# Performance work log

Measured on AMD Instinct MI355X. Metric: run time of the kernel, lower is better.

The kernel has to match this reference:

```python
import jax, jax.numpy as jnp
import numpy as np

N = 50          # n_nodes
TAU = 1.0       # sinkhorn_tau
ITERS = 5       # sinkhorn_iters
ALPHA = 1.0


def _psi_fn(x, W1, b1, W2, b2):
    # x: [B, N, F]
    h = jax.nn.leaky_relu(x @ W1 + b1)          # [B, N, H], slope 0.01 matches torch default
    M = jax.nn.leaky_relu(h @ W2 + b2)          # [B, N, N]
    P = jnp.exp(M / TAU)
    for _ in range(ITERS):                      # alternating row/col normalization
        P = P / jnp.sum(P, axis=2, keepdims=True)
        P = P / jnp.sum(P, axis=1, keepdims=True)
    return P


def _hungarian(cost):
    """O(n^3) Hungarian (shortest augmenting path, like scipy.linear_sum_assignment).
    cost: [n, n] numpy. Returns col index assigned to each row (minimizes cost)."""
    n = cost.shape[0]
    INF = 1e18
    u = np.zeros(n + 1)
    v = np.zeros(n + 1)
    p = np.zeros(n + 1, dtype=np.int64)   # p[j] = row matched to column j (1-based)
    for i in range(1, n + 1):
        p[0] = i
        j0 = 0
        minv = np.full(n + 1, INF)
        way = np.zeros(n + 1, dtype=np.int64)
        used = np.zeros(n + 1, dtype=bool)
        while True:
            used[j0] = True
            i0 = p[j0]
            cur = cost[i0 - 1, :] - u[i0] - v[1:]
            free = ~used[1:]
            better = free & (cur < minv[1:])
            mv = minv[1:]
            mv[better] = cur[better]
            way[1:][better] = j0
            cand = np.where(free, mv, INF)
            j1 = int(np.argmin(cand)) + 1
            delta = cand[j1 - 1]
            u[p[used]] += delta
            v[used] -= delta
            mv[free] -= delta
            j0 = j1
            if p[j0] == 0:
                break
        while j0 != 0:
            j1 = way[j0]
            p[j0] = p[j1]
            j0 = j1
    row_to_col = np.zeros(n, dtype=np.int64)
    for j in range(1, n + 1):
        if p[j] > 0:
            row_to_col[p[j] - 1] = j - 1
    return row_to_col


def setup_inputs() -> dict:
    key = jax.random.key(0)
    k1, k2, k3, k4, k5 = jax.random.split(key, 5)
    B, F, H = 128, 1024, 4096
    s1 = 1.0 / np.sqrt(F)
    s2 = 1.0 / np.sqrt(H)
    x = jax.random.normal(k1, (B, N, F), dtype=jnp.float32)
    W1 = jax.random.uniform(k2, (F, H), minval=-s1, maxval=s1, dtype=jnp.float32)
    b1 = jax.random.uniform(k3, (H,), minval=-s1, maxval=s1, dtype=jnp.float32)
    W2 = jax.random.uniform(k4, (H, N), minval=-s2, maxval=s2, dtype=jnp.float32)
    b2 = jax.random.uniform(k5, (N,), minval=-s2, maxval=s2, dtype=jnp.float32)
    return {"x": x, "W1": W1, "b1": b1, "W2": W2, "b2": b2, "do_round": 1}


def reference(x, W1, b1, W2, b2, do_round):
    psi = _psi_fn(x, W1, b1, W2, b2)            # [B, N, N] doubly-stochastic (approx)
    if do_round:
        batch = np.asarray(psi)
        B = batch.shape[0]
        perms_np = np.zeros((B, N, N), dtype=np.float32)
        rows = np.arange(N)
        for i in range(B):
            cols = _hungarian(-batch[i])        # maximize psi == minimize -psi
            perms_np[i, rows, cols] = 1.0
        perms = jnp.asarray(perms_np)
        dist = jnp.sum(psi * perms, axis=(1, 2)) / N   # [B]
        X = (1.0 - ALPHA) * perms + ALPHA * psi
        return (psi, perms, X, dist)
    return (psi, None, None, None)
```

## Files before the change

### kernel.cpp

```cpp
#include <hip/hip_runtime.h>

#define NMAT 50
#define BATCH 128
#define FDIM 1024
#define HDIM 4096
#define ROWS 6400
#define PSIZE 320000
#define NPART 8
#define HINF 1e18

#define WS_M_OFF   0
#define WS_XH_OFF  10240000LL
#define WS_XL_OFF  23347200LL
#define WS_W1H_OFF 36454400LL
#define WS_W1L_OFF 44843008LL
#define WS_W2H_OFF 53231616LL
#define WS_W2L_OFF 53755904LL
#define WS_H_OFF   54280192LL
#define WS_MIN     (WS_H_OFF + 128LL * HDIM * 4)

typedef __bf16 bf16x8 __attribute__((ext_vector_type(8)));
typedef short short8 __attribute__((ext_vector_type(8)));
typedef float f32x4 __attribute__((ext_vector_type(4)));
typedef unsigned short u16;
typedef unsigned int u32;

__device__ __forceinline__ float bf16_to_f32(unsigned short h) {
  return __uint_as_float(((unsigned int)h) << 16);
}
__device__ __forceinline__ unsigned short f32_to_bf16(float f) {
  unsigned int u = __float_as_uint(f);
  u += 0x7FFFu + ((u >> 16) & 1u);
  return (unsigned short)(u >> 16);
}

__device__ __forceinline__ void gload16(const u16* g, u16* l) {
  __builtin_amdgcn_global_load_lds(
      (const __attribute__((address_space(1))) unsigned int*)g,
      (__attribute__((address_space(3))) unsigned int*)l, 16, 0, 0);
}

__device__ __forceinline__ double wave_min_f64(double x) {
  union { double d; int i[2]; } u, t;
  u.d = x;
#define DPP_MIN_STEP(ctrl)                                                   \
  t.i[0] = __builtin_amdgcn_update_dpp(u.i[0], u.i[0], ctrl, 0xf, 0xf, false);\
  t.i[1] = __builtin_amdgcn_update_dpp(u.i[1], u.i[1], ctrl, 0xf, 0xf, false);\
  u.d = fmin(u.d, t.d);
  DPP_MIN_STEP(0x111)
  DPP_MIN_STEP(0x112)
  DPP_MIN_STEP(0x114)
  DPP_MIN_STEP(0x118)
  DPP_MIN_STEP(0x142)
  DPP_MIN_STEP(0x143)
#undef DPP_MIN_STEP
  union { double d; int i[2]; } r;
  r.i[0] = __builtin_amdgcn_readlane(u.i[0], 63);
  r.i[1] = __builtin_amdgcn_readlane(u.i[1], 63);
  return r.d;
}

__global__ __launch_bounds__(256) void convert_x(
    const float* __restrict__ X, u16* __restrict__ Xh, u16* __restrict__ Xl) {
  int t = threadIdx.x;
  int mt = blockIdx.x >> 5, k0b = blockIdx.x & 31;
  size_t outbase = (size_t)blockIdx.x * 4096;
#pragma unroll
  for (int it = 0; it < 2; ++it) {
    int idx = t + it * 256;
    int m = idx & 127, kg = idx >> 7;
    const float* src = X + (size_t)(mt * 128 + m) * FDIM + k0b * 32 + kg * 8;
    float4 v0 = *(const float4*)src;
    float4 v1 = *(const float4*)(src + 4);
    float f[8] = {v0.x, v0.y, v0.z, v0.w, v1.x, v1.y, v1.z, v1.w};
    unsigned short h[8], l[8];
#pragma unroll
    for (int j = 0; j < 8; ++j) {
      h[j] = f32_to_bf16(f[j]);
      l[j] = f32_to_bf16(f[j] - bf16_to_f32(h[j]));
    }
    uint4 hv, lv;
    hv.x = h[0] | ((unsigned)h[1] << 16); hv.y = h[2] | ((unsigned)h[3] << 16);
    hv.z = h[4] | ((unsigned)h[5] << 16); hv.w = h[6] | ((unsigned)h[7] << 16);
    lv.x = l[0] | ((unsigned)l[1] << 16); lv.y = l[2] | ((unsigned)l[3] << 16);
    lv.z = l[4] | ((unsigned)l[5] << 16); lv.w = l[6] | ((unsigned)l[7] << 16);
    size_t off = outbase + (size_t)(kg * 128 + m) * 8;
    *(uint4*)&Xh[off] = hv;
    *(uint4*)&Xl[off] = lv;
  }
}

__global__ __launch_bounds__(256) void convert_w1(
    const float* __restrict__ W1, u16* __restrict__ Wh, u16* __restrict__ Wl) {
  int t = threadIdx.x;
  int nt = blockIdx.x >> 5, k0b = blockIdx.x & 31;
  size_t outbase = (size_t)blockIdx.x * 4096;
#pragma unroll
  for (int it = 0; it < 2; ++it) {
    int idx = t + it * 256;
    int n = idx & 127, kg = idx >> 7;
    float f[8];
#pragma unroll
    for (int j = 0; j < 8; ++j)
      f[j] = W1[(size_t)(k0b * 32 + kg * 8 + j) * HDIM + nt * 128 + n];
    unsigned short h[8], l[8];
#pragma unroll
    for (int j = 0; j < 8; ++j) {
      h[j] = f32_to_bf16(f[j]);
      l[j] = f32_to_bf16(f[j] - bf16_to_f32(h[j]));
    }
    uint4 hv, lv;
    hv.x = h[0] | ((unsigned)h[1] << 16); hv.y = h[2] | ((unsigned)h[3] << 16);
    hv.z = h[4] | ((unsigned)h[5] << 16); hv.w = h[6] | ((unsigned)h[7] << 16);
    lv.x = l[0] | ((unsigned)l[1] << 16); lv.y = l[2] | ((unsigned)l[3] << 16);
    lv.z = l[4] | ((unsigned)l[5] << 16); lv.w = l[6] | ((unsigned)l[7] << 16);
    size_t off = outbase + (size_t)(kg * 128 + n) * 8;
    *(uint4*)&Wh[off] = hv;
    *(uint4*)&Wl[off] = lv;
  }
}

__global__ __launch_bounds__(256) void convert_w2(
    const float* __restrict__ W2, u16* __restrict__ W2h, u16* __restrict__ W2l) {
  int idx = blockIdx.x * 256 + threadIdx.x;
  int n = idx >> 12, k = idx & 4095;
  float f = (n < NMAT) ? W2[(size_t)k * NMAT + n] : 0.0f;
  unsigned short hi = f32_to_bf16(f);
  unsigned short lo = f32_to_bf16(f - bf16_to_f32(hi));
  W2h[idx] = hi;
  W2l[idx] = lo;
}

__global__ __launch_bounds__(256) void gemm1_mfma(
    const u16* __restrict__ Ah_, const u16* __restrict__ Al_,
    const u16* __restrict__ Bh_, const u16* __restrict__ Bl_,
    const float* __restrict__ b1,
    u32* __restrict__ HTout,
    int mt0, int stride) {
  __shared__ __align__(16) u16 Ah[4096];
  __shared__ __align__(16) u16 Al[4096];
  __shared__ __align__(16) u16 Bh[4096];
  __shared__ __align__(16) u16 Bl[4096];
  int t = threadIdx.x;
  int wave = t >> 6, lane = t & 63;
  int nt = blockIdx.x & 31;
  int mtl = blockIdx.x >> 5;
  int wm = wave >> 1, wn = wave & 1;
  int fr = lane & 15, fg = lane >> 4;

  f32x4 acc[4][4];
#pragma unroll
  for (int i = 0; i < 4; ++i)
#pragma unroll
    for (int j = 0; j < 4; ++j) acc[i][j] = (f32x4){0.f, 0.f, 0.f, 0.f};

  const u16* pAh = Ah_ + (size_t)(mt0 + mtl) * 32 * 4096;
  const u16* pAl = Al_ + (size_t)(mt0 + mtl) * 32 * 4096;
  const u16* pBh = Bh_ + (size_t)nt * 32 * 4096;
  const u16* pBl = Bl_ + (size_t)nt * 32 * 4096;
  int so = wave * 1024 + lane * 8;
  int ld = wave * 1024;

  for (int k0b = 0; k0b < 32; ++k0b) {
    __syncthreads();
    size_t sb = (size_t)k0b * 4096;
    gload16(pAh + sb + so,       &Ah[ld]);
    gload16(pAh + sb + so + 512, &Ah[ld + 512]);
    gload16(pAl + sb + so,       &Al[ld]);
    gload16(pAl + sb + so + 512, &Al[ld + 512]);
    gload16(pBh + sb + so,       &Bh[ld]);
    gload16(pBh + sb + so + 512, &Bh[ld + 512]);
    gload16(pBl + sb + so,       &Bl[ld]);
    gload16(pBl + sb + so + 512, &Bl[ld + 512]);
    __syncthreads();
    bf16x8 ah[4], al[4], bh[4], bl[4];
#pragma unroll
    for (int i = 0; i < 4; ++i) {
      int arow = (fg * 128 + wm * 64 + i * 16 + fr) * 8;
      ah[i] = *(const bf16x8*)&Ah[arow];
      al[i] = *(const bf16x8*)&Al[arow];
      int brow = (fg * 128 + wn * 64 + i * 16 + fr) * 8;
      bh[i] = *(const bf16x8*)&Bh[brow];
      bl[i] = *(const bf16x8*)&Bl[brow];
    }
#pragma unroll
    for (int i = 0; i < 4; ++i)
#pragma unroll
      for (int j = 0; j < 4; ++j)
        acc[i][j] = __builtin_amdgcn_mfma_f32_16x16x32_bf16(ah[i], bh[j], acc[i][j], 0, 0, 0);
#pragma unroll
    for (int i = 0; i < 4; ++i)
#pragma unroll
      for (int j = 0; j < 4; ++j)
        acc[i][j] = __builtin_amdgcn_mfma_f32_16x16x32_bf16(ah[i], bl[j], acc[i][j], 0, 0, 0);
#pragma unroll
    for (int i = 0; i < 4; ++i)
#pragma unroll
      for (int j = 0; j < 4; ++j)
        acc[i][j] = __builtin_amdgcn_mfma_f32_16x16x32_bf16(al[i], bh[j], acc[i][j], 0, 0, 0);
  }

  int colb = nt * 128 + wn * 64 + fr;
  int rowb = mtl * 128 + wm * 64 + fg * 4;
#pragma unroll
  for (int j = 0; j < 4; ++j) {
    float bias = b1[colb + j * 16];
#pragma unroll
    for (int i = 0; i < 4; ++i) {
      uint4 pk;
      u32* pp = &pk.x;
#pragma unroll
      for (int r = 0; r < 4; ++r) {
        float v = acc[i][j][r] + bias;
        v = v >= 0.0f ? v : 0.01f * v;
        unsigned short hi = f32_to_bf16(v);
        unsigned short lo = f32_to_bf16(v - bf16_to_f32(hi));
        pp[r] = ((u32)hi << 16) | lo;
      }
      *(uint4*)&HTout[(size_t)(colb + j * 16) * stride + rowb + i * 16] = pk;
    }
  }
}

__global__ __launch_bounds__(64) void gemm2_bf16(
    const u32* __restrict__ hT,
    const u16* __restrict__ W2h,
    const u16* __restrict__ W2l,
    float* __restrict__ Mpart,
    int row0, int stride) {
  int lane = threadIdx.x;
  int kz = blockIdx.y;
  int fr = lane & 15, fg = lane >> 4;

  f32x4 acc[4];
#pragma unroll
  for (int nt = 0; nt < 4; ++nt) acc[nt] = (f32x4){0.f, 0.f, 0.f, 0.f};

  const u32* hA = hT + blockIdx.x * 16 + fr;
  const int kbase = kz * 512;
  u32 hp[8];
#pragma unroll
  for (int kk = 0; kk < 8; ++kk)
    hp[kk] = hA[(size_t)(kbase + fg * 8 + kk) * stride];

  for (int ks = 0; ks < 16; ++ks) {
    int k0 = kbase + ks * 32;
    u32 hn[8];
    if (ks < 15) {
#pragma unroll
      for (int kk = 0; kk < 8; ++kk)
        hn[kk] = hA[(size_t)(k0 + 32 + fg * 8 + kk) * stride];
    }
    short8 hs, ls;
#pragma unroll
    for (int kk = 0; kk < 8; ++kk) {
      hs[kk] = (short)(hp[kk] >> 16);
      ls[kk] = (short)(hp[kk] & 0xffffu);
    }
    bf16x8 ah = *(bf16x8*)&hs;
    bf16x8 al = *(bf16x8*)&ls;
#pragma unroll
    for (int nt = 0; nt < 4; ++nt) {
      const size_t boff = (size_t)(nt * 16 + fr) * 4096 + k0 + fg * 8;
      bf16x8 bh = *(const bf16x8*)&W2h[boff];
      bf16x8 bl = *(const bf16x8*)&W2l[boff];
      acc[nt] = __builtin_amdgcn_mfma_f32_16x16x32_bf16(ah, bh, acc[nt], 0, 0, 0);
      acc[nt] = __builtin_amdgcn_mfma_f32_16x16x32_bf16(ah, bl, acc[nt], 0, 0, 0);
      acc[nt] = __builtin_amdgcn_mfma_f32_16x16x32_bf16(al, bh, acc[nt], 0, 0, 0);
    }
    if (ks < 15) {
#pragma unroll
      for (int kk = 0; kk < 8; ++kk) hp[kk] = hn[kk];
    }
  }

  float* Mout = Mpart + (size_t)kz * PSIZE;
  int rowbase = row0 + blockIdx.x * 16 + fg * 4;
#pragma unroll
  for (int nt = 0; nt < 4; ++nt) {
    int col = nt * 16 + fr;
    if (col < NMAT) {
#pragma unroll
      for (int r = 0; r < 4; ++r)
        Mout[(size_t)(rowbase + r) * NMAT + col] = acc[nt][r];
    }
  }
}

__global__ __launch_bounds__(64) void sinkhorn_hungarian(
    const float* __restrict__ Mpart, const float* __restrict__ b2,
    float* __restrict__ out_psi, float* __restrict__ out_X,
    float* __restrict__ out_perms, float* __restrict__ out_dist) {
  int b = blockIdx.x, lane = threadIdx.x;
  __shared__ double P[2500];
  __shared__ double cost[2500];
  __shared__ double rs[50];
  __shared__ double u[51];
  __shared__ int p[51];
  __shared__ int wayl[51];
  const size_t base = (size_t)b * 2500;

  for (int e = lane; e < 2500; e += 64) {
    double m = 0.0;
#pragma unroll
    for (int pz = 0; pz < NPART; ++pz)
      m += (double)Mpart[(size_t)pz * PSIZE + base + e];
    m += (double)b2[e % 50];
    m = m >= 0.0 ? m : 0.01 * m;
    P[e] = exp(m);
  }
  __syncthreads();
  for (int it = 0; it < 5; ++it) {
    if (lane < 50) { double s = 0; for (int j = 0; j < 50; ++j) s += P[lane * 50 + j]; rs[lane] = s; }
    __syncthreads();
    for (int e = lane; e < 2500; e += 64) P[e] /= rs[e / 50];
    __syncthreads();
    if (lane < 50) { double s = 0; for (int r = 0; r < 50; ++r) s += P[r * 50 + lane]; rs[lane] = s; }
    __syncthreads();
    for (int e = lane; e < 2500; e += 64) P[e] /= rs[e % 50];
    __syncthreads();
  }
  for (int e = lane; e < 2500; e += 64) {
    float f = (float)P[e];
    out_psi[base + e] = f;
    out_X[base + e] = f;
    cost[e] = -P[e];
  }
  if (lane < 51) { u[lane] = 0.0; p[lane] = 0; }
  __syncthreads();

  double v = 0.0;
  bool lactive = lane < NMAT;
  for (int i = 1; i <= NMAT; ++i) {
    bool used = false;
    int way = 0;
    int j0 = 0, j1 = 0;
    for (int guard = 0; guard < 64; ++guard) {
      if (lane == j0 - 1) used = true;
      int i0 = (j0 == 0) ? i : p[j0];
      double ui0 = u[i0];
      double cand = HINF;
      if (lactive && !used) {
        cand = cost[(i0 - 1) * NMAT + lane] - ui0 - v;
        way = j0;
      }
      double m = wave_min_f64(cand);
      unsigned long long bal = __ballot(cand == m);
      j1 = (int)__builtin_ctzll(bal) + 1;
      double delta = m;
      __syncthreads();
      if (used) { v -= delta; u[p[lane + 1]] += delta; }
      if (lane == 63) u[i] += delta;
      __syncthreads();
      j0 = j1;
      if (p[j0] == 0) break;
    }
    if (lactive) wayl[lane + 1] = way;
    __syncthreads();
    if (lane == 0) {
      int j = j1;
      for (int step = 0; step < 64 && j != 0; ++step) {
        int jw = wayl[j];
        p[j] = (jw == 0) ? i : p[jw];
        j = jw;
      }
    }
    __syncthreads();
  }

  size_t pbase = (size_t)b * 2500;
  for (int e = lane; e < 2500; e += 64) out_perms[pbase + e] = 0.0f;
  __syncthreads();
  double val = 0.0;
  if (lactive) {
    int row = p[lane + 1] - 1;
    if (row < 0) row = 0;
    if (row > 49) row = 49;
    out_perms[pbase + (size_t)row * NMAT + lane] = 1.0f;
    val = P[(size_t)row * NMAT + lane];
  }
#pragma unroll
  for (int s = 32; s > 0; s >>= 1) val += __shfl_xor(val, s, 64);
  if (lane == 0) out_dist[b] = (float)(val / (double)NMAT);
}

extern "C" void kernel_launch(void* const* d_in, const int* in_sizes, int n_in,
                              void* d_out, int out_size, void* d_ws, size_t ws_size,
                              hipStream_t stream) {
  const float* x  = (const float*)d_in[0];
  const float* W1 = (const float*)d_in[1];
  const float* b1 = (const float*)d_in[2];
  const float* W2 = (const float*)d_in[3];
  const float* b2 = (const float*)d_in[4];
  float* out = (float*)d_out;
  float* out_psi   = out;
  float* out_perms = out + PSIZE;
  float* out_X     = out + 2 * PSIZE;
  float* out_dist  = out + 3 * PSIZE;

  if (ws_size < (size_t)WS_MIN) return;

  char* ws = (char*)d_ws;
  float* Mpart = (float*)(ws + WS_M_OFF);
  u16* Xh  = (u16*)(ws + WS_XH_OFF);
  u16* Xl  = (u16*)(ws + WS_XL_OFF);
  u16* W1h = (u16*)(ws + WS_W1H_OFF);
  u16* W1l = (u16*)(ws + WS_W1L_OFF);
  u16* W2h = (u16*)(ws + WS_W2H_OFF);
  u16* W2l = (u16*)(ws + WS_W2L_OFF);
  u32* hbuf = (u32*)(ws + WS_H_OFF);
  long long avail = (long long)ws_size - WS_H_OFF;
  int max_rows = (int)(avail / (HDIM * 4));
  max_rows = (max_rows / 128) * 128;
  if (max_rows > ROWS) max_rows = ROWS;

  hipLaunchKernelGGL(convert_x, dim3(1600), dim3(256), 0, stream, x, Xh, Xl);
  hipLaunchKernelGGL(convert_w1, dim3(1024), dim3(256), 0, stream, W1, W1h, W1l);
  hipLaunchKernelGGL(convert_w2, dim3(1024), dim3(256), 0, stream, W2, W2h, W2l);

  for (int r0 = 0; r0 < ROWS; r0 += max_rows) {
    int rows = (ROWS - r0 < max_rows) ? (ROWS - r0) : max_rows;
    hipLaunchKernelGGL(gemm1_mfma, dim3((rows / 128) * 32), dim3(256), 0, stream,
                       Xh, Xl, W1h, W1l, b1, hbuf, r0 / 128, rows);
    hipLaunchKernelGGL(gemm2_bf16, dim3(rows / 16, NPART), dim3(64), 0, stream,
                       hbuf, W2h, W2l, Mpart, r0, rows);
  }
  hipLaunchKernelGGL(sinkhorn_hungarian, dim3(BATCH), dim3(64), 0, stream,
                     Mpart, b2, out_psi, out_X, out_perms, out_dist);
}
```

Baseline: 474.6 us.

## Keep Hungarian duals in registers and double gemm2 K-split with deeper prefetch

Result: faster. 460.8 us (-2.9%).

```diff
diff --git a/kernel.cpp b/kernel.cpp
--- a/kernel.cpp
+++ b/kernel.cpp
@@ -6,17 +6,17 @@
 #define HDIM 4096
 #define ROWS 6400
 #define PSIZE 320000
-#define NPART 8
+#define NPART 16
 #define HINF 1e18
 
 #define WS_M_OFF   0
-#define WS_XH_OFF  10240000LL
-#define WS_XL_OFF  23347200LL
-#define WS_W1H_OFF 36454400LL
-#define WS_W1L_OFF 44843008LL
-#define WS_W2H_OFF 53231616LL
-#define WS_W2L_OFF 53755904LL
-#define WS_H_OFF   54280192LL
+#define WS_XH_OFF  20480000LL
+#define WS_XL_OFF  33587200LL
+#define WS_W1H_OFF 46694400LL
+#define WS_W1L_OFF 55083008LL
+#define WS_W2H_OFF 63471616LL
+#define WS_W2L_OFF 63995904LL
+#define WS_H_OFF   64520192LL
 #define WS_MIN     (WS_H_OFF + 128LL * HDIM * 4)
 
 typedef __bf16 bf16x8 __attribute__((ext_vector_type(8)));
@@ -60,6 +60,14 @@
   return r.d;
 }
 
+__device__ __forceinline__ double readlane_f64(double x, int l) {
+  union { double d; int i2[2]; } a, b;
+  a.d = x;
+  b.i2[0] = __builtin_amdgcn_readlane(a.i2[0], l);
+  b.i2[1] = __builtin_amdgcn_readlane(a.i2[1], l);
+  return b.d;
+}
+
 __global__ __launch_bounds__(256) void convert_x(
     const float* __restrict__ X, u16* __restrict__ Xh, u16* __restrict__ Xl) {
   int t = threadIdx.x;
@@ -237,19 +245,22 @@
   for (int nt = 0; nt < 4; ++nt) acc[nt] = (f32x4){0.f, 0.f, 0.f, 0.f};
 
   const u32* hA = hT + blockIdx.x * 16 + fr;
-  const int kbase = kz * 512;
-  u32 hp[8];
+  const int kbase = kz * 256;
+  u32 hp[8], hn[8];
 #pragma unroll
   for (int kk = 0; kk < 8; ++kk)
     hp[kk] = hA[(size_t)(kbase + fg * 8 + kk) * stride];
-
-  for (int ks = 0; ks < 16; ++ks) {
+#pragma unroll
+  for (int kk = 0; kk < 8; ++kk)
+    hn[kk] = hA[(size_t)(kbase + 32 + fg * 8 + kk) * stride];
+
+  for (int ks = 0; ks < 8; ++ks) {
     int k0 = kbase + ks * 32;
-    u32 hn[8];
-    if (ks < 15) {
+    u32 h2[8];
+    if (ks < 6) {
 #pragma unroll
       for (int kk = 0; kk < 8; ++kk)
-        hn[kk] = hA[(size_t)(k0 + 32 + fg * 8 + kk) * stride];
+        h2[kk] = hA[(size_t)(k0 + 64 + fg * 8 + kk) * stride];
     }
     short8 hs, ls;
 #pragma unroll
@@ -268,9 +279,13 @@
       acc[nt] = __builtin_amdgcn_mfma_f32_16x16x32_bf16(ah, bl, acc[nt], 0, 0, 0);
       acc[nt] = __builtin_amdgcn_mfma_f32_16x16x32_bf16(al, bh, acc[nt], 0, 0, 0);
     }
-    if (ks < 15) {
+    if (ks < 7) {
 #pragma unroll
       for (int kk = 0; kk < 8; ++kk) hp[kk] = hn[kk];
+    }
+    if (ks < 6) {
+#pragma unroll
+      for (int kk = 0; kk < 8; ++kk) hn[kk] = h2[kk];
     }
   }
 
@@ -332,13 +347,17 @@
   double v = 0.0;
   bool lactive = lane < NMAT;
   for (int i = 1; i <= NMAT; ++i) {
+    int pc = (lane <= 50) ? p[lane] : 0;
+    double uc = (lane < 50) ? u[lane + 1] : 0.0;
     bool used = false;
     int way = 0;
     int j0 = 0, j1 = 0;
+    double uacc = 0.0, total = 0.0;
     for (int guard = 0; guard < 64; ++guard) {
       if (lane == j0 - 1) used = true;
-      int i0 = (j0 == 0) ? i : p[j0];
-      double ui0 = u[i0];
+      int j0u = __builtin_amdgcn_readfirstlane(j0);
+      int i0 = (j0u == 0) ? i : __builtin_amdgcn_readlane(pc, j0u);
+      double ui0 = readlane_f64(uc, i0 - 1);
       double cand = HINF;
       if (lactive && !used) {
         cand = cost[(i0 - 1) * NMAT + lane] - ui0 - v;
@@ -347,14 +366,14 @@
       double m = wave_min_f64(cand);
       unsigned long long bal = __ballot(cand == m);
       j1 = (int)__builtin_ctzll(bal) + 1;
-      double delta = m;
-      __syncthreads();
-      if (used) { v -= delta; u[p[lane + 1]] += delta; }
-      if (lane == 63) u[i] += delta;
-      __syncthreads();
+      if (used) { v -= m; uacc += m; }
+      total += m;
       j0 = j1;
-      if (p[j0] == 0) break;
-    }
+      int j1u = __builtin_amdgcn_readfirstlane(j0);
+      if (__builtin_amdgcn_readlane(pc, j1u) == 0) break;
+    }
+    if (used && lactive) u[p[lane + 1]] += uacc;
+    if (lane == 63) u[i] += total;
     if (lactive) wayl[lane + 1] = way;
     __syncthreads();
     if (lane == 0) {
```
